# Optimization experiments

Measured on AMD Instinct MI355X. Metric: run time of the kernel, lower is better.

## Reference

```python
import jax, jax.numpy as jnp
import numpy as np

EMB_DIM = 1024
N_HEADS = 16
HEAD_DIM = 64
B, S = 4, 2048


def setup_inputs() -> dict:
    key = jax.random.key(0)
    k_x, k_qkv, k_out = jax.random.split(key, 3)
    hd = N_HEADS * HEAD_DIM
    # torch Linear(in, out, bias=False): y = x @ W.T, W:[out, in]. Store transposed [in, out].
    x = jax.random.normal(k_x, (B, S, EMB_DIM), dtype=jnp.float32)
    W_qkv = jax.random.normal(k_qkv, (EMB_DIM, 3 * hd), dtype=jnp.float32) * (EMB_DIM ** -0.5)
    W_out = jax.random.normal(k_out, (hd, EMB_DIM), dtype=jnp.float32) * (hd ** -0.5)
    return {"x": x, "W_qkv": W_qkv, "W_out": W_out}


def reference(x, W_qkv, W_out):
    Bv, Sv, _ = x.shape
    hd = N_HEADS * HEAD_DIM
    scale = HEAD_DIM ** -0.5
    qkv = x @ W_qkv  # [B, S, 3*H*D]
    q, k, v = jnp.split(qkv, 3, axis=-1)
    # [B, S, H, D] -> [B, H, S, D]
    reshape_heads = lambda t: t.reshape(Bv, Sv, N_HEADS, HEAD_DIM).transpose(0, 2, 1, 3)
    q, k, v = reshape_heads(q), reshape_heads(k), reshape_heads(v)
    scores = scale * jnp.einsum("bhsd,bhtd->bhst", q, k)
    a = jax.nn.softmax(scores, axis=-1)
    z = jnp.einsum("bhst,bhtd->bhsd", a, v)  # [B, H, S, D]
    # FAITHFUL to original bug: reshape [B,H,S,D] directly to [B,S,H*D] (no head transpose back)
    z = z.reshape(Bv, Sv, hd)
    return z @ W_out
```

## Files before the change

kernel.cpp:

```cpp
#include <hip/hip_runtime.h>
#include <hip/hip_bf16.h>
#include <cstdint>
#include <cstddef>

#define B_   4
#define S_   2048
#define EMB_ 1024
#define NH_  16
#define HD_  64
#define M1_  (B_*S_)

typedef __attribute__((ext_vector_type(8))) short short8v;
typedef __attribute__((ext_vector_type(4))) float f32x4;
typedef unsigned short u16;

__device__ __forceinline__ u16 f2bf(float f) {
  uint32_t u = __builtin_bit_cast(uint32_t, f);
  uint32_t lsb = (u >> 16) & 1u;
  u += 0x7fffu + lsb;
  return (u16)(u >> 16);
}

__device__ __forceinline__ void gll16(const void* g, void* lds) {
  __builtin_amdgcn_global_load_lds(
      (const __attribute__((address_space(1))) void*)g,
      (__attribute__((address_space(3))) void*)lds, 16, 0, 0);
}

__global__ void k_cvt(const float* __restrict__ in, u16* __restrict__ out, int n) {
  int idx = blockIdx.x * blockDim.x + threadIdx.x;
  int stride = gridDim.x * blockDim.x;
  for (int i = idx * 4; i < n; i += stride * 4) {
    float4 v = *reinterpret_cast<const float4*>(in + i);
    ushort4 o = make_ushort4(f2bf(v.x), f2bf(v.y), f2bf(v.z), f2bf(v.w));
    *reinterpret_cast<ushort4*>(out + i) = o;
  }
}

__global__ void k_transpose(const float* __restrict__ in, u16* __restrict__ out,
                            int R, int C) {
  __shared__ float tile[64][65];
  const int c0 = blockIdx.x * 64, r0 = blockIdx.y * 64;
  const int tc = threadIdx.x & 63;
  const int t4 = threadIdx.x >> 6;
#pragma unroll
  for (int i = 0; i < 16; ++i) {
    int r = i * 4 + t4;
    tile[r][tc] = in[(size_t)(r0 + r) * C + c0 + tc];
  }
  __syncthreads();
#pragma unroll
  for (int i = 0; i < 16; ++i) {
    int cc = i * 4 + t4;
    out[(size_t)(c0 + cc) * R + r0 + tc] = f2bf(tile[tc][cc]);
  }
}

template <int EPI>
__global__ __launch_bounds__(256, 2)
void k_gemm(const u16* __restrict__ A, const u16* __restrict__ Bt,
            float* __restrict__ Cf,
            u16* __restrict__ qb, u16* __restrict__ kb, u16* __restrict__ vtb,
            int K, int Nt) {
  __shared__ u16 As[128 * 64];
  __shared__ u16 Bs[128 * 64];
  const int tid = threadIdx.x;
  const int wid = tid >> 6, lane = tid & 63;
  const int l15 = lane & 15, g = lane >> 4;
  const int wr = wid >> 1, wc = wid & 1;
  const int bm0 = blockIdx.x << 7, bn0 = blockIdx.y << 7;
  f32x4 acc[4][4] = {};
  const char* Asc = (const char*)As;
  const char* Bsc = (const char*)Bs;
  const int nK = K >> 6;
  for (int kt = 0; kt < nK; ++kt) {
    const int k0 = kt << 6;
#pragma unroll
    for (int it = 0; it < 4; ++it) {
      int ch = it * 256 + tid;
      int row = ch >> 3, cb = (ch & 7) << 3;
      gll16(A + (size_t)(bm0 + row) * K + k0 + cb,
            (char*)As + (size_t)(it * 256 + wid * 64) * 16);
    }
#pragma unroll
    for (int it = 0; it < 4; ++it) {
      int ch = it * 256 + tid;
      int row = ch >> 3, cb = (ch & 7) << 3;
      gll16(Bt + (size_t)(bn0 + row) * K + k0 + cb,
            (char*)Bs + (size_t)(it * 256 + wid * 64) * 16);
    }
    __syncthreads();
#pragma unroll
    for (int ks = 0; ks < 2; ++ks) {
      short8v af[4], bfv[4];
#pragma unroll
      for (int mi = 0; mi < 4; ++mi)
        af[mi] = *(const short8v*)(Asc + ((size_t)(wr * 64 + mi * 16 + l15) * 64 + ks * 32 + g * 8) * 2);
#pragma unroll
      for (int ni = 0; ni < 4; ++ni)
        bfv[ni] = *(const short8v*)(Bsc + ((size_t)(wc * 64 + ni * 16 + l15) * 64 + ks * 32 + g * 8) * 2);
#pragma unroll
      for (int mi = 0; mi < 4; ++mi)
#pragma unroll
        for (int ni = 0; ni < 4; ++ni)
          acc[mi][ni] = __builtin_amdgcn_mfma_f32_16x16x32_bf16(af[mi], bfv[ni], acc[mi][ni], 0, 0, 0);
    }
    __syncthreads();
  }
#pragma unroll
  for (int mi = 0; mi < 4; ++mi)
#pragma unroll
    for (int ni = 0; ni < 4; ++ni)
#pragma unroll
      for (int r = 0; r < 4; ++r) {
        int row = bm0 + wr * 64 + mi * 16 + g * 4 + r;
        int col = bn0 + wc * 64 + ni * 16 + l15;
        float v = acc[mi][ni][r];
        if (EPI == 0) {
          Cf[(size_t)row * Nt + col] = v;
        } else {
          int part = col >> 10;
          int h = (col & 1023) >> 6;
          int d = col & 63;
          int b = row >> 11, s = row & 2047;
          size_t bh = (size_t)(b * NH_ + h);
          if (part == 0)       qb[(bh * S_ + s) * HD_ + d] = f2bf(v * 0.125f);
          else if (part == 1)  kb[(bh * S_ + s) * HD_ + d] = f2bf(v);
          else                 vtb[(bh * HD_ + d) * S_ + s] = f2bf(v);
        }
      }
}

__global__ __launch_bounds__(256, 2)
void k_attn(const u16* __restrict__ qb, const u16* __restrict__ kb,
            const u16* __restrict__ vtb, u16* __restrict__ zb) {
  __shared__ char smem[65536];
  char* Ks = smem;
  char* Vs = smem + 16384;
  char* Ps = smem + 32768;
  const int tid = threadIdx.x;
  const int wid = tid >> 6, lane = tid & 63;
  const int l15 = lane & 15, g = lane >> 4;
  const int bh = blockIdx.x >> 4;
  const int qt = blockIdx.x & 15;
  const u16* qh = qb + (size_t)bh * S_ * HD_;
  const u16* kh = kb + (size_t)bh * S_ * HD_;
  const u16* vh = vtb + (size_t)bh * HD_ * S_;
  u16* zh = zb + (size_t)bh * S_ * HD_;
  const int qrow0 = qt * 128 + wid * 32;

  short8v qf[2][2];
#pragma unroll
  for (int mi = 0; mi < 2; ++mi)
#pragma unroll
    for (int ks = 0; ks < 2; ++ks)
      qf[mi][ks] = *(const short8v*)(qh + (size_t)(qrow0 + mi * 16 + l15) * HD_ + ks * 32 + g * 8);

  f32x4 of[2][4] = {};
  float mst[2][4], lst[2][4];
#pragma unroll
  for (int mi = 0; mi < 2; ++mi)
#pragma unroll
    for (int r = 0; r < 4; ++r) { mst[mi][r] = -__builtin_inff(); lst[mi][r] = 0.f; }
  char* pw = Ps + wid * 8192;

  for (int t0 = 0; t0 < S_; t0 += 128) {
#pragma unroll
    for (int it = 0; it < 4; ++it) {
      int ch = it * 256 + tid;
      int trow = ch >> 3;
      int sb = ((ch & 7) << 4) ^ ((trow & 7) << 4);
      gll16(kh + (size_t)(t0 + trow) * HD_ + (sb >> 1),
            Ks + (size_t)(it * 256 + wid * 64) * 16);
    }
#pragma unroll
    for (int it = 0; it < 4; ++it) {
      int ch = it * 256 + tid;
      int d = ch >> 4;
      int sb = ((ch & 15) << 4) ^ ((d & 7) << 4);
      gll16(vh + (size_t)d * S_ + t0 + (sb >> 1),
            Vs + (size_t)(it * 256 + wid * 64) * 16);
    }
    __syncthreads();

    f32x4 sf[2][8];
#pragma unroll
    for (int mi = 0; mi < 2; ++mi)
#pragma unroll
      for (int nj = 0; nj < 8; ++nj) sf[mi][nj] = (f32x4){0.f, 0.f, 0.f, 0.f};
#pragma unroll
    for (int ks = 0; ks < 2; ++ks) {
#pragma unroll
      for (int nj = 0; nj < 8; ++nj) {
        int trow = nj * 16 + l15;
        int cb = (ks * 64 + g * 16) ^ ((trow & 7) << 4);
        short8v kf = *(const short8v*)(Ks + trow * 128 + cb);
        sf[0][nj] = __builtin_amdgcn_mfma_f32_16x16x32_bf16(qf[0][ks], kf, sf[0][nj], 0, 0, 0);
        sf[1][nj] = __builtin_amdgcn_mfma_f32_16x16x32_bf16(qf[1][ks], kf, sf[1][nj], 0, 0, 0);
      }
    }

#pragma unroll
    for (int mi = 0; mi < 2; ++mi)
#pragma unroll
      for (int r = 0; r < 4; ++r) {
        float mx = sf[mi][0][r];
#pragma unroll
        for (int nj = 1; nj < 8; ++nj) mx = fmaxf(mx, sf[mi][nj][r]);
#pragma unroll
        for (int off = 1; off < 16; off <<= 1) mx = fmaxf(mx, __shfl_xor(mx, off, 64));
        float mold = mst[mi][r];
        float mnew = fmaxf(mold, mx);
        float alpha = __expf(mold - mnew);
        mst[mi][r] = mnew;
        float rs = 0.f;
#pragma unroll
        for (int nj = 0; nj < 8; ++nj) {
          float p = __expf(sf[mi][nj][r] - mnew);
          sf[mi][nj][r] = p;
          rs += p;
        }
#pragma unroll
        for (int off = 1; off < 16; off <<= 1) rs += __shfl_xor(rs, off, 64);
        lst[mi][r] = lst[mi][r] * alpha + rs;
#pragma unroll
        for (int dj = 0; dj < 4; ++dj) of[mi][dj][r] *= alpha;
        int prow = mi * 16 + g * 4 + r;
        int swz = ((prow >> 2) & 3) << 5;
#pragma unroll
        for (int nj = 0; nj < 8; ++nj) {
          int cb = (nj * 32 + l15 * 2) ^ swz;
          *(u16*)(pw + prow * 256 + cb) = f2bf(sf[mi][nj][r]);
        }
      }

#pragma unroll
    for (int ks = 0; ks < 4; ++ks) {
      short8v pf[2];
#pragma unroll
      for (int mi = 0; mi < 2; ++mi) {
        int prow = mi * 16 + l15;
        int cb = (ks * 64 + g * 16) ^ (((prow >> 2) & 3) << 5);
        pf[mi] = *(const short8v*)(pw + prow * 256 + cb);
      }
#pragma unroll
      for (int dj = 0; dj < 4; ++dj) {
        int d = dj * 16 + l15;
        int cb = (ks * 64 + g * 16) ^ ((d & 7) << 4);
        short8v vf = *(const short8v*)(Vs + d * 256 + cb);
        of[0][dj] = __builtin_amdgcn_mfma_f32_16x16x32_bf16(pf[0], vf, of[0][dj], 0, 0, 0);
        of[1][dj] = __builtin_amdgcn_mfma_f32_16x16x32_bf16(pf[1], vf, of[1][dj], 0, 0, 0);
      }
    }
    __syncthreads();
  }

#pragma unroll
  for (int mi = 0; mi < 2; ++mi)
#pragma unroll
    for (int dj = 0; dj < 4; ++dj)
#pragma unroll
      for (int r = 0; r < 4; ++r) {
        int srow = qrow0 + mi * 16 + g * 4 + r;
        int col = dj * 16 + l15;
        float v = of[mi][dj][r] / lst[mi][r];
        zh[(size_t)srow * HD_ + col] = f2bf(v);
      }
}

extern "C" void kernel_launch(void* const* d_in, const int* in_sizes, int n_in,
                              void* d_out, int out_size, void* d_ws, size_t ws_size,
                              hipStream_t stream) {
  const float* x    = (const float*)d_in[0];
  const float* Wqkv = (const float*)d_in[1];
  const float* Wout = (const float*)d_in[2];
  float* out = (float*)d_out;
  char* ws = (char*)d_ws;
  u16* xb    = (u16*)(ws);
  u16* wqkvT = (u16*)(ws + 16777216);
  u16* woutT = (u16*)(ws + 23068672);
  u16* qbuf  = (u16*)(ws + 25165824);
  u16* kbuf  = (u16*)(ws + 41943040);
  u16* vtbuf = (u16*)(ws + 58720256);
  u16* zbuf  = (u16*)(ws + 75497472);

  k_cvt<<<2048, 256, 0, stream>>>(x, xb, M1_ * EMB_);
  k_transpose<<<dim3(3 * EMB_ / 64, EMB_ / 64), 256, 0, stream>>>(Wqkv, wqkvT, EMB_, 3 * EMB_);
  k_transpose<<<dim3(EMB_ / 64, EMB_ / 64), 256, 0, stream>>>(Wout, woutT, EMB_, EMB_);
  k_gemm<1><<<dim3(M1_ / 128, 3 * EMB_ / 128), 256, 0, stream>>>(
      xb, wqkvT, nullptr, qbuf, kbuf, vtbuf, EMB_, 3 * EMB_);
  k_attn<<<dim3(B_ * NH_ * 16), 256, 0, stream>>>(qbuf, kbuf, vtbuf, zbuf);
  k_gemm<0><<<dim3(M1_ / 128, EMB_ / 128), 256, 0, stream>>>(
      zbuf, woutT, out, nullptr, nullptr, nullptr, EMB_, EMB_);
}
```

Measured before the change: 366.2 us.

## Transpose attention MFMA operands so each lane owns one query row; use exp2

Swaps the MFMA operand order (K·Q and V·P) so the score and output accumulators are transposed and each lane holds a single query row. Row max and sum then need only two cross-lane shuffles instead of four per reduction. Folds log2(e) into the Q scale so softmax can use exp2f, and writes P to LDS as packed 32-bit bf16 pairs instead of scalar 16-bit stores. The output write becomes strided per lane, and the swizzle is simplified to one precomputed value.

```diff
diff --git a/kernel.cpp b/kernel.cpp
--- a/kernel.cpp
+++ b/kernel.cpp
@@ -14,11 +14,17 @@
 typedef __attribute__((ext_vector_type(4))) float f32x4;
 typedef unsigned short u16;
 
+#define QSCALE 0.18033688011112042f
+
 __device__ __forceinline__ u16 f2bf(float f) {
   uint32_t u = __builtin_bit_cast(uint32_t, f);
   uint32_t lsb = (u >> 16) & 1u;
   u += 0x7fffu + lsb;
   return (u16)(u >> 16);
+}
+
+__device__ __forceinline__ uint32_t pack2(float a, float b) {
+  return (uint32_t)f2bf(a) | ((uint32_t)f2bf(b) << 16);
 }
 
 __device__ __forceinline__ void gll16(const void* g, void* lds) {
@@ -124,7 +130,7 @@
           int d = col & 63;
           int b = row >> 11, s = row & 2047;
           size_t bh = (size_t)(b * NH_ + h);
-          if (part == 0)       qb[(bh * S_ + s) * HD_ + d] = f2bf(v * 0.125f);
+          if (part == 0)       qb[(bh * S_ + s) * HD_ + d] = f2bf(v * QSCALE);
           else if (part == 1)  kb[(bh * S_ + s) * HD_ + d] = f2bf(v);
           else                 vtb[(bh * HD_ + d) * S_ + s] = f2bf(v);
         }
@@ -148,6 +154,7 @@
   const u16* vh = vtb + (size_t)bh * HD_ * S_;
   u16* zh = zb + (size_t)bh * S_ * HD_;
   const int qrow0 = qt * 128 + wid * 32;
+  const int swz = (l15 & 7) << 4;
 
   short8v qf[2][2];
 #pragma unroll
@@ -157,11 +164,8 @@
       qf[mi][ks] = *(const short8v*)(qh + (size_t)(qrow0 + mi * 16 + l15) * HD_ + ks * 32 + g * 8);
 
   f32x4 of[2][4] = {};
-  float mst[2][4], lst[2][4];
-#pragma unroll
-  for (int mi = 0; mi < 2; ++mi)
-#pragma unroll
-    for (int r = 0; r < 4; ++r) { mst[mi][r] = -__builtin_inff(); lst[mi][r] = 0.f; }
+  float mst[2] = {-__builtin_inff(), -__builtin_inff()};
+  float lst[2] = {0.f, 0.f};
   char* pw = Ps + wid * 8192;
 
   for (int t0 = 0; t0 < S_; t0 += 128) {
@@ -192,80 +196,73 @@
     for (int ks = 0; ks < 2; ++ks) {
 #pragma unroll
       for (int nj = 0; nj < 8; ++nj) {
-        int trow = nj * 16 + l15;
-        int cb = (ks * 64 + g * 16) ^ ((trow & 7) << 4);
-        short8v kf = *(const short8v*)(Ks + trow * 128 + cb);
-        sf[0][nj] = __builtin_amdgcn_mfma_f32_16x16x32_bf16(qf[0][ks], kf, sf[0][nj], 0, 0, 0);
-        sf[1][nj] = __builtin_amdgcn_mfma_f32_16x16x32_bf16(qf[1][ks], kf, sf[1][nj], 0, 0, 0);
-      }
-    }
-
-#pragma unroll
-    for (int mi = 0; mi < 2; ++mi)
-#pragma unroll
-      for (int r = 0; r < 4; ++r) {
-        float mx = sf[mi][0][r];
-#pragma unroll
-        for (int nj = 1; nj < 8; ++nj) mx = fmaxf(mx, sf[mi][nj][r]);
-#pragma unroll
-        for (int off = 1; off < 16; off <<= 1) mx = fmaxf(mx, __shfl_xor(mx, off, 64));
-        float mold = mst[mi][r];
-        float mnew = fmaxf(mold, mx);
-        float alpha = __expf(mold - mnew);
-        mst[mi][r] = mnew;
-        float rs = 0.f;
-#pragma unroll
-        for (int nj = 0; nj < 8; ++nj) {
-          float p = __expf(sf[mi][nj][r] - mnew);
-          sf[mi][nj][r] = p;
-          rs += p;
-        }
-#pragma unroll
-        for (int off = 1; off < 16; off <<= 1) rs += __shfl_xor(rs, off, 64);
-        lst[mi][r] = lst[mi][r] * alpha + rs;
-#pragma unroll
-        for (int dj = 0; dj < 4; ++dj) of[mi][dj][r] *= alpha;
-        int prow = mi * 16 + g * 4 + r;
-        int swz = ((prow >> 2) & 3) << 5;
-#pragma unroll
-        for (int nj = 0; nj < 8; ++nj) {
-          int cb = (nj * 32 + l15 * 2) ^ swz;
-          *(u16*)(pw + prow * 256 + cb) = f2bf(sf[mi][nj][r]);
-        }
-      }
+        int cb = (ks * 64 + g * 16) ^ swz;
+        short8v kf = *(const short8v*)(Ks + (nj * 16 + l15) * 128 + cb);
+        sf[0][nj] = __builtin_amdgcn_mfma_f32_16x16x32_bf16(kf, qf[0][ks], sf[0][nj], 0, 0, 0);
+        sf[1][nj] = __builtin_amdgcn_mfma_f32_16x16x32_bf16(kf, qf[1][ks], sf[1][nj], 0, 0, 0);
+      }
+    }
+
+#pragma unroll
+    for (int mi = 0; mi < 2; ++mi) {
+      f32x4 m4 = sf[mi][0];
+#pragma unroll
+      for (int nj = 1; nj < 8; ++nj) {
+#pragma unroll
+        for (int e = 0; e < 4; ++e) m4[e] = fmaxf(m4[e], sf[mi][nj][e]);
+      }
+      float mx = fmaxf(fmaxf(m4[0], m4[1]), fmaxf(m4[2], m4[3]));
+      mx = fmaxf(mx, __shfl_xor(mx, 16, 64));
+      mx = fmaxf(mx, __shfl_xor(mx, 32, 64));
+      float mnew = fmaxf(mst[mi], mx);
+      float al = exp2f(mst[mi] - mnew);
+#pragma unroll
+      for (int dj = 0; dj < 4; ++dj) of[mi][dj] *= al;
+      lst[mi] *= al;
+      mst[mi] = mnew;
+      f32x4 rs4 = (f32x4){0.f, 0.f, 0.f, 0.f};
+#pragma unroll
+      for (int nj = 0; nj < 8; ++nj) {
+        f32x4 p4;
+#pragma unroll
+        for (int e = 0; e < 4; ++e) p4[e] = exp2f(sf[mi][nj][e] - mnew);
+        rs4 += p4;
+        char* paddr = pw + (mi * 16 + l15) * 256 + ((nj * 32 + g * 8) ^ swz);
+        *(uint32_t*)(paddr)     = pack2(p4[0], p4[1]);
+        *(uint32_t*)(paddr + 4) = pack2(p4[2], p4[3]);
+      }
+      float rs = (rs4[0] + rs4[1]) + (rs4[2] + rs4[3]);
+      rs += __shfl_xor(rs, 16, 64);
+      rs += __shfl_xor(rs, 32, 64);
+      lst[mi] += rs;
+    }
 
 #pragma unroll
     for (int ks = 0; ks < 4; ++ks) {
-      short8v pf[2];
-#pragma unroll
-      for (int mi = 0; mi < 2; ++mi) {
-        int prow = mi * 16 + l15;
-        int cb = (ks * 64 + g * 16) ^ (((prow >> 2) & 3) << 5);
-        pf[mi] = *(const short8v*)(pw + prow * 256 + cb);
-      }
+      short8v pbm[2];
+#pragma unroll
+      for (int mi = 0; mi < 2; ++mi)
+        pbm[mi] = *(const short8v*)(pw + (mi * 16 + l15) * 256 + ((ks * 64 + g * 16) ^ swz));
 #pragma unroll
       for (int dj = 0; dj < 4; ++dj) {
-        int d = dj * 16 + l15;
-        int cb = (ks * 64 + g * 16) ^ ((d & 7) << 4);
-        short8v vf = *(const short8v*)(Vs + d * 256 + cb);
-        of[0][dj] = __builtin_amdgcn_mfma_f32_16x16x32_bf16(pf[0], vf, of[0][dj], 0, 0, 0);
-        of[1][dj] = __builtin_amdgcn_mfma_f32_16x16x32_bf16(pf[1], vf, of[1][dj], 0, 0, 0);
-      }
-    }
-    __syncthreads();
-  }
-
-#pragma unroll
-  for (int mi = 0; mi < 2; ++mi)
+        short8v vf = *(const short8v*)(Vs + (dj * 16 + l15) * 256 + ((ks * 64 + g * 16) ^ swz));
+        of[0][dj] = __builtin_amdgcn_mfma_f32_16x16x32_bf16(vf, pbm[0], of[0][dj], 0, 0, 0);
+        of[1][dj] = __builtin_amdgcn_mfma_f32_16x16x32_bf16(vf, pbm[1], of[1][dj], 0, 0, 0);
+      }
+    }
+    __syncthreads();
+  }
+
+#pragma unroll
+  for (int mi = 0; mi < 2; ++mi) {
+    float inv = 1.0f / lst[mi];
 #pragma unroll
     for (int dj = 0; dj < 4; ++dj)
 #pragma unroll
-      for (int r = 0; r < 4; ++r) {
-        int srow = qrow0 + mi * 16 + g * 4 + r;
-        int col = dj * 16 + l15;
-        float v = of[mi][dj][r] / lst[mi][r];
-        zh[(size_t)srow * HD_ + col] = f2bf(v);
-      }
+      for (int r = 0; r < 4; ++r)
+        zh[(size_t)(qrow0 + mi * 16 + l15) * HD_ + dj * 16 + g * 4 + r] =
+            f2bf(of[mi][dj][r] * inv);
+  }
 }
 
 extern "C" void kernel_launch(void* const* d_in, const int* in_sizes, int n_in,
```

Result: no change. 365.1 us (-0.3%).
